# Kernel tuning notes

Hardware: AMD Instinct MI355X
Metric: run time of the kernel (lower is better)

Reference implementation:

```python
import jax, jax.numpy as jnp
from jax import lax
import numpy as np

B, N, CIN, COUT, HID = 16, 4096, 64, 128, 128
RATIO, K = 0.25, 32
M = int(N * RATIO)  # 1024 sampled centroids per cloud


def setup_inputs() -> dict:
    key = jax.random.key(0)
    ks = jax.random.split(key, 6)
    s = 0.02
    return {
        "x": jax.random.normal(ks[0], (B, N, CIN), jnp.float32),
        "pos": jax.random.normal(ks[1], (B, N, 3), jnp.float32),
        "W1": jax.random.normal(ks[2], (CIN + 3, HID), jnp.float32) * s,
        "b1": jnp.zeros((HID,), jnp.float32),
        "W2": jax.random.normal(ks[3], (HID, COUT), jnp.float32) * s,
        "b2": jnp.zeros((COUT,), jnp.float32),
        "Wlin": jax.random.normal(ks[4], (CIN, COUT), jnp.float32) * s,
        "blin": jnp.zeros((COUT,), jnp.float32),
    }


def mish(v):
    return v * jnp.tanh(jax.nn.softplus(v))


def fps(pc, m):
    # Farthest point sampling (deterministic start at index 0, as PyG with random_start=False).
    n = pc.shape[0]

    def step(carry, _):
        mind, last = carry
        d = jnp.sum((pc - pc[last]) ** 2, axis=-1)  # [N]
        mind = jnp.minimum(mind, d)
        nxt = jnp.argmax(mind).astype(jnp.int32)
        return (mind, nxt), nxt

    init = (jnp.full((n,), np.inf, pc.dtype), jnp.int32(0))
    _, rest = lax.scan(step, init, None, length=m - 1)
    return jnp.concatenate([jnp.zeros((1,), jnp.int32), rest])  # [M]


def reference(x, pos, W1, b1, W2, b2, Wlin, blin):
    def per_cloud(xc, pc):
        # xc: [N,CIN], pc: [N,3]
        idx = fps(pc, M)                                        # [M]
        q = pc[idx]                                             # [M,3] sampled centroids
        d2 = jnp.sum((q[:, None, :] - pc[None, :, :]) ** 2, -1)  # [M,N]
        _, nbr = lax.top_k(-d2, K)                              # [M,K] knn indices
        rel = pc[nbr] - q[:, None, :]                           # [M,K,3]
        h = jnp.concatenate([xc[nbr], rel], axis=-1)            # [M,K,CIN+3]
        h = mish(h @ W1 + b1)                                   # local_nn layer 1
        h = h @ W2 + b2                                         # [M,K,COUT]
        agg = jnp.max(h, axis=1)                                # PointNetConv max aggregation
        out = agg + xc[idx] @ Wlin + blin                       # residual skip via self.lin
        return out, q

    x_out, pos_out = jax.vmap(per_cloud)(x, pos)
    return x_out, pos_out
```

## Files before the change

### kernel.cpp

```cpp
#include <hip/hip_runtime.h>
#include <hip/hip_bf16.h>

constexpr int B    = 16;
constexpr int N    = 4096;
constexpr int CIN  = 64;
constexpr int COUT = 128;
constexpr int M    = 1024;
constexpr int K    = 32;

constexpr int K1  = 96;
constexpr int LDH = 136;

typedef __attribute__((ext_vector_type(8))) short short8;
typedef __attribute__((ext_vector_type(4))) float f32x4;
typedef __attribute__((ext_vector_type(2))) float f32x2;

static __device__ __forceinline__ unsigned short f2bf(float f) {
  unsigned u = __float_as_uint(f);
  unsigned r = (u + 0x7FFFu + ((u >> 16) & 1u)) >> 16;
  return (unsigned short)r;
}

static __device__ __forceinline__ float fast_mish(float v) {
  float u = __expf(v);
  float s = u * (u + 2.0f);
  float t = s / (s + 2.0f);
  return (v > 60.f) ? v : v * t;
}

template <int CTRL, int RM>
static __device__ __forceinline__ unsigned dpp_umax_step(unsigned x) {
  int o = __builtin_amdgcn_update_dpp((int)x, (int)x, CTRL, RM, 0xF, false);
  unsigned u = (unsigned)o;
  return x > u ? x : u;
}
static __device__ __forceinline__ unsigned wave_umax(unsigned x) {
  x = dpp_umax_step<0x111, 0xF>(x);
  x = dpp_umax_step<0x112, 0xF>(x);
  x = dpp_umax_step<0x114, 0xF>(x);
  x = dpp_umax_step<0x118, 0xF>(x);
  x = dpp_umax_step<0x142, 0xA>(x);
  x = dpp_umax_step<0x143, 0xC>(x);
  return (unsigned)__builtin_amdgcn_readlane((int)x, 63);
}

static __device__ __forceinline__ unsigned long long umax64(unsigned long long a,
                                                            unsigned long long b) {
  return a > b ? a : b;
}

__global__ __launch_bounds__(512) void fps8_kernel(const float* __restrict__ pos,
                                                   int* __restrict__ idx_out,
                                                   float* __restrict__ pout,
                                                   float* __restrict__ pos4) {
#pragma clang fp contract(off)
  const int b   = blockIdx.x;
  const int tid = threadIdx.x;
  __shared__ float sp[N][4];
  __shared__ unsigned long long skey[2][8];
  const float* p = pos + (size_t)b * (N * 3);
  float* p4 = pos4 + (size_t)b * N * 4;

  f32x2 px2[4], py2[4], pz2[4];
  float mind[8];
#pragma unroll
  for (int j = 0; j < 8; j++) {
    const int n = tid + j * 512;
    const float x = p[3 * n + 0];
    const float y = p[3 * n + 1];
    const float z = p[3 * n + 2];
    px2[j >> 1][j & 1] = x;
    py2[j >> 1][j & 1] = y;
    pz2[j >> 1][j & 1] = z;
    mind[j] = __builtin_inff();
    f32x4 v;
    v[0] = x; v[1] = y; v[2] = z; v[3] = 0.f;
    *(f32x4*)(&sp[n][0]) = v;
    *(f32x4*)(p4 + 4 * n) = v;
  }
  float qx = p[0], qy = p[1], qz = p[2];
  if (tid == 0) {
    idx_out[b * M + 0] = 0;
    pout[(size_t)(b * M + 0) * 3 + 0] = qx;
    pout[(size_t)(b * M + 0) * 3 + 1] = qy;
    pout[(size_t)(b * M + 0) * 3 + 2] = qz;
  }
  __syncthreads();

  const int wv = tid >> 6, lane = tid & 63;
  for (int t = 1; t < M; t++) {
    const f32x2 nqx = {-qx, -qx};
    const f32x2 nqy = {-qy, -qy};
    const f32x2 nqz = {-qz, -qz};
    float bv = -1.f;
    unsigned bn = 0;
#pragma unroll
    for (int k = 0; k < 4; k++) {
      f32x2 dx = px2[k] + nqx;
      f32x2 dy = py2[k] + nqy;
      f32x2 dz = pz2[k] + nqz;
      f32x2 s = (dx * dx + dy * dy) + dz * dz;
      const float mi0 = fminf(mind[2 * k + 0], s.x);
      mind[2 * k + 0] = mi0;
      bool c0 = mi0 > bv;
      bv = c0 ? mi0 : bv;
      bn = c0 ? (unsigned)(tid + (2 * k + 0) * 512) : bn;
      const float mi1 = fminf(mind[2 * k + 1], s.y);
      mind[2 * k + 1] = mi1;
      bool c1 = mi1 > bv;
      bv = c1 ? mi1 : bv;
      bn = c1 ? (unsigned)(tid + (2 * k + 1) * 512) : bn;
    }
    const unsigned vb = __float_as_uint(bv);
    const unsigned wb = wave_umax(vb);
    unsigned tk = (vb == wb) ? ~bn : 0u;
    tk = wave_umax(tk);
    const int par = t & 1;
    if (lane == 0) skey[par][wv] = ((unsigned long long)wb << 32) | tk;
    __syncthreads();
    const unsigned long long k0 = skey[par][0];
    const unsigned long long k1 = skey[par][1];
    const unsigned long long k2 = skey[par][2];
    const unsigned long long k3 = skey[par][3];
    const unsigned long long k4 = skey[par][4];
    const unsigned long long k5 = skey[par][5];
    const unsigned long long k6 = skey[par][6];
    const unsigned long long k7 = skey[par][7];
    const unsigned long long bb =
        umax64(umax64(umax64(k0, k1), umax64(k2, k3)),
               umax64(umax64(k4, k5), umax64(k6, k7)));
    const unsigned n = ~(unsigned)bb;
    const f32x4 qv = *(const f32x4*)(&sp[n][0]);
    qx = qv[0];
    qy = qv[1];
    qz = qv[2];
    if (tid == 0) {
      idx_out[b * M + t] = (int)n;
      pout[(size_t)(b * M + t) * 3 + 0] = qx;
      pout[(size_t)(b * M + t) * 3 + 1] = qy;
      pout[(size_t)(b * M + t) * 3 + 2] = qz;
    }
  }
}

__global__ __launch_bounds__(256) void knn5_kernel(const float* __restrict__ pos4,
                                                   const int* __restrict__ idx,
                                                   int* __restrict__ nbr) {
#pragma clang fp contract(off)
  const int wv   = threadIdx.x >> 6;
  const int lane = threadIdx.x & 63;
  const int cent = blockIdx.x * 4 + wv;
  const int b = cent >> 10;
  const float* p4 = pos4 + (size_t)b * N * 4;
  const int sel = idx[cent];
  const f32x4 q = *(const f32x4*)(p4 + 4 * sel);
  const f32x2 nqx = {-q[0], -q[0]};
  const f32x2 nqy = {-q[1], -q[1]};
  const f32x2 nqz = {-q[2], -q[2]};

  float d[64];
#pragma unroll
  for (int jj = 0; jj < 32; jj++) {
    const f32x4 v0 = *(const f32x4*)(p4 + 4 * ((2 * jj + 0) * 64 + lane));
    const f32x4 v1 = *(const f32x4*)(p4 + 4 * ((2 * jj + 1) * 64 + lane));
    f32x2 vx = {v0[0], v1[0]};
    f32x2 vy = {v0[1], v1[1]};
    f32x2 vz = {v0[2], v1[2]};
    f32x2 dx = vx + nqx;
    f32x2 dy = vy + nqy;
    f32x2 dz = vz + nqz;
    f32x2 s = (dx * dx + dy * dy) + dz * dz;
    d[2 * jj + 0] = s.x;
    d[2 * jj + 1] = s.y;
  }
  float gv[8];
  int gj[8];
#pragma unroll
  for (int g = 0; g < 8; g++) {
    gv[g] = __builtin_inff();
    gj[g] = 8 * g;
#pragma unroll
    for (int e = 0; e < 8; e++) {
      const int j = 8 * g + e;
      bool c = d[j] < gv[g];
      gv[g] = c ? d[j] : gv[g];
      gj[g] = c ? j : gj[g];
    }
  }

  int* out = nbr + (size_t)cent * K;
  for (int r = 0; r < K; r++) {
    float bv = __builtin_inff();
    int bj = 0;
#pragma unroll
    for (int g = 0; g < 8; g++) {
      bool c = gv[g] < bv;
      bv = c ? gv[g] : bv;
      bj = c ? gj[g] : bj;
    }
    const unsigned bn = (unsigned)(bj * 64 + lane);
    const unsigned nb = ~__float_as_uint(bv);
    const unsigned wnb = wave_umax(nb);
    unsigned tk = (nb == wnb) ? (0xFFFFFFFFu - bn) : 0u;
    tk = wave_umax(tk);
    const unsigned wn = 0xFFFFFFFFu - tk;
    if (lane == 0) out[r] = (int)wn;

    const int wj = (int)(wn >> 6);
    const int wl = (int)(wn & 63);
    const int wg = wj >> 3;
#pragma unroll
    for (int g = 0; g < 8; g++) {
      if (g == wg) {
#pragma unroll
        for (int e = 0; e < 8; e++) {
          if (8 * g + e == wj) {
            if (lane == wl) d[8 * g + e] = __builtin_inff();
          }
        }
        float nv = __builtin_inff();
        int nj = 8 * g;
#pragma unroll
        for (int e = 0; e < 8; e++) {
          const int j = 8 * g + e;
          bool c = d[j] < nv;
          nv = c ? d[j] : nv;
          nj = c ? j : nj;
        }
        gv[g] = nv;
        gj[g] = nj;
      }
    }
  }
}

__global__ __launch_bounds__(256) void prep_weights(const float* __restrict__ W1,
                                                    const float* __restrict__ W2,
                                                    unsigned short* __restrict__ W1t,
                                                    unsigned short* __restrict__ W2t) {
  const int n = blockIdx.x;
  const int t = threadIdx.x;
  if (t < K1) {
    W1t[n * K1 + t] = (t < 67) ? f2bf(W1[t * 128 + n]) : (unsigned short)0;
  } else if (t < K1 + 128) {
    int k = t - K1;
    W2t[n * 128 + k] = f2bf(W2[k * 128 + n]);
  }
}

__global__ __launch_bounds__(256) void mlp3_kernel(
    const float* __restrict__ x, const float* __restrict__ pos,
    const unsigned short* __restrict__ W1t, const unsigned short* __restrict__ W2t,
    const float* __restrict__ b1, const float* __restrict__ b2,
    const float* __restrict__ Wlin, const float* __restrict__ blin,
    const int* __restrict__ idx, const int* __restrict__ nbr,
    float* __restrict__ xout) {
  __shared__ unsigned short sA2[4][32][LDH];
  const int tid  = threadIdx.x;
  const int wv   = tid >> 6;
  const int lane = tid & 63;
  const int lrow = lane & 15;
  const int g    = lane >> 4;
  const int cent = blockIdx.x * 4 + wv;
  const int b    = cent >> 10;
  const int sel  = idx[cent];
  const float* pb = pos + (size_t)b * (N * 3);
  const float qx = pb[3 * sel + 0], qy = pb[3 * sel + 1], qz = pb[3 * sel + 2];
  unsigned short* A2 = &sA2[wv][0][0];

  const int n0 = nbr[(size_t)cent * K + lrow];
  const int n1 = nbr[(size_t)cent * K + 16 + lrow];

  short8 a0[3], a1[3];
  {
    const float* xr0 = x + ((size_t)b * N + n0) * CIN;
    const float* xr1 = x + ((size_t)b * N + n1) * CIN;
#pragma unroll
    for (int kc = 0; kc < 2; kc++) {
      const int k0 = kc * 32 + g * 8;
      f32x4 u0 = *(const f32x4*)(xr0 + k0);
      f32x4 u1 = *(const f32x4*)(xr0 + k0 + 4);
      f32x4 v0 = *(const f32x4*)(xr1 + k0);
      f32x4 v1 = *(const f32x4*)(xr1 + k0 + 4);
      short8 ha, hb;
#pragma unroll
      for (int e = 0; e < 4; e++) {
        ha[e] = (short)f2bf(u0[e]);
        ha[e + 4] = (short)f2bf(u1[e]);
        hb[e] = (short)f2bf(v0[e]);
        hb[e + 4] = (short)f2bf(v1[e]);
      }
      a0[kc] = ha;
      a1[kc] = hb;
    }
    short8 z = {};
    a0[2] = z;
    a1[2] = z;
    if (g == 0) {
      float r0x = pb[3 * n0 + 0] - qx, r0y = pb[3 * n0 + 1] - qy, r0z = pb[3 * n0 + 2] - qz;
      float r1x = pb[3 * n1 + 0] - qx, r1y = pb[3 * n1 + 1] - qy, r1z = pb[3 * n1 + 2] - qz;
      a0[2][0] = (short)f2bf(r0x); a0[2][1] = (short)f2bf(r0y); a0[2][2] = (short)f2bf(r0z);
      a1[2][0] = (short)f2bf(r1x); a1[2][1] = (short)f2bf(r1y); a1[2][2] = (short)f2bf(r1z);
    }
  }

#pragma unroll 2
  for (int nt = 0; nt < 8; nt++) {
    const unsigned short* w1r = W1t + (size_t)(nt * 16 + lrow) * K1 + g * 8;
    f32x4 c0 = {}, c1 = {};
#pragma unroll
    for (int kc = 0; kc < 3; kc++) {
      short8 bfr = *(const short8*)(w1r + kc * 32);
      c0 = __builtin_amdgcn_mfma_f32_16x16x32_bf16(a0[kc], bfr, c0, 0, 0, 0);
      c1 = __builtin_amdgcn_mfma_f32_16x16x32_bf16(a1[kc], bfr, c1, 0, 0, 0);
    }
    const int colI = nt * 16 + lrow;
    const float bb = b1[colI];
#pragma unroll
    for (int reg = 0; reg < 4; reg++) {
      const int row = g * 4 + reg;
      A2[row * LDH + colI] = f2bf(fast_mish(c0[reg] + bb));
      A2[(16 + row) * LDH + colI] = f2bf(fast_mish(c1[reg] + bb));
    }
  }

  f32x4 xq[4];
  {
    const float* xs = x + ((size_t)b * N + sel) * CIN + g * 16;
#pragma unroll
    for (int v = 0; v < 4; v++) xq[v] = *(const f32x4*)(xs + 4 * v);
  }

#pragma unroll 2
  for (int nt = 0; nt < 8; nt++) {
    const unsigned short* w2r = W2t + (size_t)(nt * 16 + lrow) * 128 + g * 8;
    f32x4 c0 = {}, c1 = {};
#pragma unroll
    for (int kc = 0; kc < 4; kc++) {
      short8 af0 = *(const short8*)(A2 + lrow * LDH + kc * 32 + g * 8);
      short8 af1 = *(const short8*)(A2 + (16 + lrow) * LDH + kc * 32 + g * 8);
      short8 bfr = *(const short8*)(w2r + kc * 32);
      c0 = __builtin_amdgcn_mfma_f32_16x16x32_bf16(af0, bfr, c0, 0, 0, 0);
      c1 = __builtin_amdgcn_mfma_f32_16x16x32_bf16(af1, bfr, c1, 0, 0, 0);
    }
    float pm = fmaxf(fmaxf(fmaxf(c0[0], c0[1]), fmaxf(c0[2], c0[3])),
                     fmaxf(fmaxf(c1[0], c1[1]), fmaxf(c1[2], c1[3])));
    pm = fmaxf(pm, __shfl_xor(pm, 16, 64));
    pm = fmaxf(pm, __shfl_xor(pm, 32, 64));
    const int j = nt * 16 + lrow;
    float s = 0.f;
#pragma unroll
    for (int e = 0; e < 16; e++) {
      s += xq[e >> 2][e & 3] * Wlin[(g * 16 + e) * 128 + j];
    }
    s += __shfl_xor(s, 16, 64);
    s += __shfl_xor(s, 32, 64);
    if (g == 0) {
      xout[(size_t)cent * 128 + j] = pm + b2[j] + s + blin[j];
    }
  }
}

extern "C" void kernel_launch(void* const* d_in, const int* in_sizes, int n_in,
                              void* d_out, int out_size, void* d_ws, size_t ws_size,
                              hipStream_t stream) {
  const float* x    = (const float*)d_in[0];
  const float* pos  = (const float*)d_in[1];
  const float* W1   = (const float*)d_in[2];
  const float* b1   = (const float*)d_in[3];
  const float* W2   = (const float*)d_in[4];
  const float* b2   = (const float*)d_in[5];
  const float* Wlin = (const float*)d_in[6];
  const float* blin = (const float*)d_in[7];

  float* out  = (float*)d_out;
  float* xout = out;
  float* pout = out + (size_t)B * M * COUT;

  char* ws = (char*)d_ws;
  int* idx            = (int*)ws;
  int* nbr            = (int*)(ws + 65536);
  unsigned short* W1t = (unsigned short*)(ws + 65536 + 2097152);
  unsigned short* W2t = (unsigned short*)(ws + 65536 + 2097152 + 24576);
  float* pos4         = (float*)(ws + 65536 + 2097152 + 24576 + 32768);

  prep_weights<<<dim3(128), dim3(256), 0, stream>>>(W1, W2, W1t, W2t);
  fps8_kernel<<<dim3(B), dim3(512), 0, stream>>>(pos, idx, pout, pos4);
  knn5_kernel<<<dim3(B * M / 4), dim3(256), 0, stream>>>(pos4, idx, nbr);
  mlp3_kernel<<<dim3(B * M / 4), dim3(256), 0, stream>>>(
      x, pos, W1t, W2t, b1, b2, Wlin, blin, idx, nbr, xout);
}
```

Baseline: 941.9 us.

## Stage point cloud in LDS for kNN, transpose MLP1 MFMA, use rcp in mish

The kNN kernel now uses 512-thread blocks that cooperatively copy the whole cloud's padded positions into 64KB of shared memory, then compute distances from LDS instead of re-reading global memory per wave. The MLP kernel swaps the MFMA operand order in layer 1 so each lane holds four consecutive hidden columns, allowing vectorized bias loads and 4-wide LDS stores of the activations. Mish's division is replaced by a hardware reciprocal, and relative positions are read from the padded float4 buffer. The 64KB shared allocation limits kNN occupancy, and the reciprocal slightly changes numerics.

Result: no change. 935.8 us (-0.7%).

```diff
diff --git a/kernel.cpp b/kernel.cpp
--- a/kernel.cpp
+++ b/kernel.cpp
@@ -12,6 +12,7 @@
 constexpr int LDH = 136;
 
 typedef __attribute__((ext_vector_type(8))) short short8;
+typedef __attribute__((ext_vector_type(4))) short short4v;
 typedef __attribute__((ext_vector_type(4))) float f32x4;
 typedef __attribute__((ext_vector_type(2))) float f32x2;
 
@@ -24,7 +25,10 @@
 static __device__ __forceinline__ float fast_mish(float v) {
   float u = __expf(v);
   float s = u * (u + 2.0f);
-  float t = s / (s + 2.0f);
+  float den = s + 2.0f;
+  float r;
+  asm("v_rcp_f32 %0, %1" : "=v"(r) : "v"(den));
+  float t = s * r;
   return (v > 60.f) ? v : v * t;
 }
 
@@ -143,97 +147,6 @@
   }
 }
 
-__global__ __launch_bounds__(256) void knn5_kernel(const float* __restrict__ pos4,
-                                                   const int* __restrict__ idx,
-                                                   int* __restrict__ nbr) {
-#pragma clang fp contract(off)
-  const int wv   = threadIdx.x >> 6;
-  const int lane = threadIdx.x & 63;
-  const int cent = blockIdx.x * 4 + wv;
-  const int b = cent >> 10;
-  const float* p4 = pos4 + (size_t)b * N * 4;
-  const int sel = idx[cent];
-  const f32x4 q = *(const f32x4*)(p4 + 4 * sel);
-  const f32x2 nqx = {-q[0], -q[0]};
-  const f32x2 nqy = {-q[1], -q[1]};
-  const f32x2 nqz = {-q[2], -q[2]};
-
-  float d[64];
-#pragma unroll
-  for (int jj = 0; jj < 32; jj++) {
-    const f32x4 v0 = *(const f32x4*)(p4 + 4 * ((2 * jj + 0) * 64 + lane));
-    const f32x4 v1 = *(const f32x4*)(p4 + 4 * ((2 * jj + 1) * 64 + lane));
-    f32x2 vx = {v0[0], v1[0]};
-    f32x2 vy = {v0[1], v1[1]};
-    f32x2 vz = {v0[2], v1[2]};
-    f32x2 dx = vx + nqx;
-    f32x2 dy = vy + nqy;
-    f32x2 dz = vz + nqz;
-    f32x2 s = (dx * dx + dy * dy) + dz * dz;
-    d[2 * jj + 0] = s.x;
-    d[2 * jj + 1] = s.y;
-  }
-  float gv[8];
-  int gj[8];
-#pragma unroll
-  for (int g = 0; g < 8; g++) {
-    gv[g] = __builtin_inff();
-    gj[g] = 8 * g;
-#pragma unroll
-    for (int e = 0; e < 8; e++) {
-      const int j = 8 * g + e;
-      bool c = d[j] < gv[g];
-      gv[g] = c ? d[j] : gv[g];
-      gj[g] = c ? j : gj[g];
-    }
-  }
-
-  int* out = nbr + (size_t)cent * K;
-  for (int r = 0; r < K; r++) {
-    float bv = __builtin_inff();
-    int bj = 0;
-#pragma unroll
-    for (int g = 0; g < 8; g++) {
-      bool c = gv[g] < bv;
-      bv = c ? gv[g] : bv;
-      bj = c ? gj[g] : bj;
-    }
-    const unsigned bn = (unsigned)(bj * 64 + lane);
-    const unsigned nb = ~__float_as_uint(bv);
-    const unsigned wnb = wave_umax(nb);
-    unsigned tk = (nb == wnb) ? (0xFFFFFFFFu - bn) : 0u;
-    tk = wave_umax(tk);
-    const unsigned wn = 0xFFFFFFFFu - tk;
-    if (lane == 0) out[r] = (int)wn;
-
-    const int wj = (int)(wn >> 6);
-    const int wl = (int)(wn & 63);
-    const int wg = wj >> 3;
-#pragma unroll
-    for (int g = 0; g < 8; g++) {
-      if (g == wg) {
-#pragma unroll
-        for (int e = 0; e < 8; e++) {
-          if (8 * g + e == wj) {
-            if (lane == wl) d[8 * g + e] = __builtin_inff();
-          }
-        }
-        float nv = __builtin_inff();
-        int nj = 8 * g;
-#pragma unroll
-        for (int e = 0; e < 8; e++) {
-          const int j = 8 * g + e;
-          bool c = d[j] < nv;
-          nv = c ? d[j] : nv;
-          nj = c ? j : nj;
-        }
-        gv[g] = nv;
-        gj[g] = nj;
-      }
-    }
-  }
-}
-
 __global__ __launch_bounds__(256) void prep_weights(const float* __restrict__ W1,
                                                     const float* __restrict__ W2,
                                                     unsigned short* __restrict__ W1t,
@@ -248,8 +161,106 @@
   }
 }
 
-__global__ __launch_bounds__(256) void mlp3_kernel(
-    const float* __restrict__ x, const float* __restrict__ pos,
+__global__ __launch_bounds__(512) void knn6_kernel(const float* __restrict__ pos4,
+                                                   const int* __restrict__ idx,
+                                                   int* __restrict__ nbr) {
+#pragma clang fp contract(off)
+  __shared__ float sp4[N * 4];
+  const int tid  = threadIdx.x;
+  const int wv   = tid >> 6;
+  const int lane = tid & 63;
+  const int cent = blockIdx.x * 8 + wv;
+  const int b = cent >> 10;
+  const float* p4 = pos4 + (size_t)b * N * 4;
+  for (int i = tid; i < N; i += 512) {
+    *(f32x4*)(sp4 + 4 * i) = *(const f32x4*)(p4 + 4 * i);
+  }
+  __syncthreads();
+
+  const int sel = idx[cent];
+  const f32x4 q = *(const f32x4*)(sp4 + 4 * sel);
+  const f32x2 nqx = {-q[0], -q[0]};
+  const f32x2 nqy = {-q[1], -q[1]};
+  const f32x2 nqz = {-q[2], -q[2]};
+
+  float d[64];
+#pragma unroll
+  for (int jj = 0; jj < 32; jj++) {
+    const f32x4 v0 = *(const f32x4*)(sp4 + 4 * ((2 * jj + 0) * 64 + lane));
+    const f32x4 v1 = *(const f32x4*)(sp4 + 4 * ((2 * jj + 1) * 64 + lane));
+    f32x2 vx = {v0[0], v1[0]};
+    f32x2 vy = {v0[1], v1[1]};
+    f32x2 vz = {v0[2], v1[2]};
+    f32x2 dx = vx + nqx;
+    f32x2 dy = vy + nqy;
+    f32x2 dz = vz + nqz;
+    f32x2 s = (dx * dx + dy * dy) + dz * dz;
+    d[2 * jj + 0] = s.x;
+    d[2 * jj + 1] = s.y;
+  }
+  float gv[8];
+  int gj[8];
+#pragma unroll
+  for (int g = 0; g < 8; g++) {
+    gv[g] = __builtin_inff();
+    gj[g] = 8 * g;
+#pragma unroll
+    for (int e = 0; e < 8; e++) {
+      const int j = 8 * g + e;
+      bool c = d[j] < gv[g];
+      gv[g] = c ? d[j] : gv[g];
+      gj[g] = c ? j : gj[g];
+    }
+  }
+
+  int* out = nbr + (size_t)cent * K;
+  for (int r = 0; r < K; r++) {
+    float bv = __builtin_inff();
+    int bj = 0;
+#pragma unroll
+    for (int g = 0; g < 8; g++) {
+      bool c = gv[g] < bv;
+      bv = c ? gv[g] : bv;
+      bj = c ? gj[g] : bj;
+    }
+    const unsigned bn = (unsigned)(bj * 64 + lane);
+    const unsigned nb = ~__float_as_uint(bv);
+    const unsigned wnb = wave_umax(nb);
+    unsigned tk = (nb == wnb) ? (0xFFFFFFFFu - bn) : 0u;
+    tk = wave_umax(tk);
+    const unsigned wn = 0xFFFFFFFFu - tk;
+    if (lane == 0) out[r] = (int)wn;
+
+    const int wj = (int)(wn >> 6);
+    const int wl = (int)(wn & 63);
+    const int wg = wj >> 3;
+#pragma unroll
+    for (int g = 0; g < 8; g++) {
+      if (g == wg) {
+#pragma unroll
+        for (int e = 0; e < 8; e++) {
+          if (8 * g + e == wj) {
+            if (lane == wl) d[8 * g + e] = __builtin_inff();
+          }
+        }
+        float nv = __builtin_inff();
+        int nj = 8 * g;
+#pragma unroll
+        for (int e = 0; e < 8; e++) {
+          const int j = 8 * g + e;
+          bool c = d[j] < nv;
+          nv = c ? d[j] : nv;
+          nj = c ? j : nj;
+        }
+        gv[g] = nv;
+        gj[g] = nj;
+      }
+    }
+  }
+}
+
+__global__ __launch_bounds__(256) void mlp4_kernel(
+    const float* __restrict__ x, const float* __restrict__ pos4,
     const unsigned short* __restrict__ W1t, const unsigned short* __restrict__ W2t,
     const float* __restrict__ b1, const float* __restrict__ b2,
     const float* __restrict__ Wlin, const float* __restrict__ blin,
@@ -261,12 +272,13 @@
   const int lane = tid & 63;
   const int lrow = lane & 15;
   const int g    = lane >> 4;
+  unsigned short* A2 = &sA2[wv][0][0];
   const int cent = blockIdx.x * 4 + wv;
   const int b    = cent >> 10;
   const int sel  = idx[cent];
-  const float* pb = pos + (size_t)b * (N * 3);
-  const float qx = pb[3 * sel + 0], qy = pb[3 * sel + 1], qz = pb[3 * sel + 2];
-  unsigned short* A2 = &sA2[wv][0][0];
+  const float* p4 = pos4 + (size_t)b * N * 4;
+  const f32x4 q = *(const f32x4*)(p4 + 4 * sel);
+  const float qx = q[0], qy = q[1], qz = q[2];
 
   const int n0 = nbr[(size_t)cent * K + lrow];
   const int n1 = nbr[(size_t)cent * K + 16 + lrow];
@@ -297,8 +309,8 @@
     a0[2] = z;
     a1[2] = z;
     if (g == 0) {
-      float r0x = pb[3 * n0 + 0] - qx, r0y = pb[3 * n0 + 1] - qy, r0z = pb[3 * n0 + 2] - qz;
-      float r1x = pb[3 * n1 + 0] - qx, r1y = pb[3 * n1 + 1] - qy, r1z = pb[3 * n1 + 2] - qz;
+      float r0x = p4[4 * n0 + 0] - qx, r0y = p4[4 * n0 + 1] - qy, r0z = p4[4 * n0 + 2] - qz;
+      float r1x = p4[4 * n1 + 0] - qx, r1y = p4[4 * n1 + 1] - qy, r1z = p4[4 * n1 + 2] - qz;
       a0[2][0] = (short)f2bf(r0x); a0[2][1] = (short)f2bf(r0y); a0[2][2] = (short)f2bf(r0z);
       a1[2][0] = (short)f2bf(r1x); a1[2][1] = (short)f2bf(r1y); a1[2][2] = (short)f2bf(r1z);
     }
@@ -310,18 +322,20 @@
     f32x4 c0 = {}, c1 = {};
 #pragma unroll
     for (int kc = 0; kc < 3; kc++) {
-      short8 bfr = *(const short8*)(w1r + kc * 32);
-      c0 = __builtin_amdgcn_mfma_f32_16x16x32_bf16(a0[kc], bfr, c0, 0, 0, 0);
-      c1 = __builtin_amdgcn_mfma_f32_16x16x32_bf16(a1[kc], bfr, c1, 0, 0, 0);
-    }
-    const int colI = nt * 16 + lrow;
-    const float bb = b1[colI];
+      short8 afr = *(const short8*)(w1r + kc * 32);
+      c0 = __builtin_amdgcn_mfma_f32_16x16x32_bf16(afr, a0[kc], c0, 0, 0, 0);
+      c1 = __builtin_amdgcn_mfma_f32_16x16x32_bf16(afr, a1[kc], c1, 0, 0, 0);
+    }
+    const int kbase = nt * 16 + g * 4;
+    const f32x4 bb = *(const f32x4*)(b1 + kbase);
+    short4v h0, h1;
 #pragma unroll
     for (int reg = 0; reg < 4; reg++) {
-      const int row = g * 4 + reg;
-      A2[row * LDH + colI] = f2bf(fast_mish(c0[reg] + bb));
-      A2[(16 + row) * LDH + colI] = f2bf(fast_mish(c1[reg] + bb));
-    }
+      h0[reg] = (short)f2bf(fast_mish(c0[reg] + bb[reg]));
+      h1[reg] = (short)f2bf(fast_mish(c1[reg] + bb[reg]));
+    }
+    *(short4v*)(A2 + lrow * LDH + kbase) = h0;
+    *(short4v*)(A2 + (16 + lrow) * LDH + kbase) = h1;
   }
 
   f32x4 xq[4];
@@ -386,7 +400,7 @@
 
   prep_weights<<<dim3(128), dim3(256), 0, stream>>>(W1, W2, W1t, W2t);
   fps8_kernel<<<dim3(B), dim3(512), 0, stream>>>(pos, idx, pout, pos4);
-  knn5_kernel<<<dim3(B * M / 4), dim3(256), 0, stream>>>(pos4, idx, nbr);
-  mlp3_kernel<<<dim3(B * M / 4), dim3(256), 0, stream>>>(
-      x, pos, W1t, W2t, b1, b2, Wlin, blin, idx, nbr, xout);
-}
+  knn6_kernel<<<dim3(B * M / 8), dim3(512), 0, stream>>>(pos4, idx, nbr);
+  mlp4_kernel<<<dim3(B * M / 4), dim3(256), 0, stream>>>(
+      x, pos4, W1t, W2t, b1, b2, Wlin, blin, idx, nbr, xout);
+}
```
